# Optimization experiments

Hardware: AMD Instinct MI355X
Metric: run time of the kernel (lower is better)

The kernel has to match this reference:

```python
import jax, jax.numpy as jnp
import numpy as np
from jax import lax

B, J, I = 32, 48, 48          # batch, target len, source len
W = 2                          # target_window_size
CTX = 2 * W + 1                # 5
E, H = 128, 256                # embedding_size, hidden_units
VT, VS = 32000, 32000          # target / source vocab
S = 2 * J                      # HMM states (word + null)


def setup_inputs() -> dict:
    key = jax.random.key(0)
    ks = jax.random.split(key, 12)
    inp = {
        "target_embedding": jax.random.normal(ks[0], (VT, E), jnp.float32) * 0.02,
        "W_bridge": jax.random.normal(ks[1], (E * CTX, E), jnp.float32) * 0.02,
        "W_hidden": jax.random.normal(ks[2], (E, H), jnp.float32) * 0.02,
        "b_hidden": jnp.zeros((H,), jnp.float32),
        "W_vocab": jax.random.normal(ks[3], (H, VS), jnp.float32) * 0.02,
        "b_vocab": jnp.zeros((VS,), jnp.float32),
        "transition": jax.random.uniform(ks[4], (B, S, S), jnp.float32, 0.01, 1.0),
        "initial_transition": jax.random.uniform(ks[5], (B, S), jnp.float32, 0.01, 1.0),
        "targets_ctx": jax.random.randint(ks[6], (B, J * CTX), 0, VT, jnp.int32),
        "targets_ctx_null": jax.random.randint(ks[7], (B, J * CTX), 0, VT, jnp.int32),
        "sources": jax.random.randint(ks[8], (B, I), 0, VS, jnp.int32),
    }
    return inp


def _emission(emb, Wb, Wh, bh, Wv, bv, ctx_ids, sources):
    # embedding lookup + context reshape: [B, J*CTX, E] -> [B, J, CTX*E]
    x = emb[ctx_ids].reshape(ctx_ids.shape[0], -1, CTX * E)
    h = jnp.tanh(jnp.einsum('bjc,ce,eh->bjh', x, Wb, Wh) + bh)  # bridge+hidden
    probs = jax.nn.softmax(h @ Wv + bv, axis=-1)                # [B, J, VS]
    # per-example gather of source token columns -> [B, J, I]
    return jax.vmap(lambda p, s: p[:, s])(probs, sources)


def _forward_backward(pi, A, em):
    # pi [B,S], A [B,S,S], em [B,S,I]; scaled HMM forward-backward
    e = jnp.moveaxis(em, 2, 0)  # [I, B, S]
    a0 = pi * e[0]
    c0 = a0.sum(-1, keepdims=True)
    a0 = a0 / c0

    def fstep(a, ei):
        an = jnp.einsum('bs,bst->bt', a, A) * ei
        c = an.sum(-1, keepdims=True)
        an = an / c
        return an, (an, c)

    _, (alphas, cs) = lax.scan(fstep, a0, e[1:])
    alphas = jnp.concatenate([a0[None], alphas], 0)          # [I,B,S]
    cs = jnp.concatenate([c0[None], cs], 0)                  # [I,B,1]

    def bstep(b, inp):
        ei, ci = inp
        bn = jnp.einsum('bst,bt->bs', A, ei * b) / ci
        return bn, bn

    bI = jnp.ones_like(a0)
    _, betas_rev = lax.scan(bstep, bI, (e[1:][::-1], cs[1:][::-1]))
    betas = jnp.concatenate([betas_rev[::-1], bI[None]], 0)  # [I,B,S]

    gamma = alphas * betas                                   # state posteriors
    loglik = jnp.log(cs[..., 0]).sum(0)                      # [B]
    return jnp.moveaxis(gamma, 0, 2), loglik


def reference(target_embedding, W_bridge, W_hidden, b_hidden, W_vocab, b_vocab,
              transition, initial_transition, targets_ctx, targets_ctx_null, sources):
    em_word = _emission(target_embedding, W_bridge, W_hidden, b_hidden,
                        W_vocab, b_vocab, targets_ctx, sources)       # [B,J,I]
    em_null = _emission(target_embedding, W_bridge, W_hidden, b_hidden,
                        W_vocab, b_vocab, targets_ctx_null, sources)  # [B,J,I]
    emission = jnp.concatenate([em_word, em_null], axis=1)            # [B,2J,I]
    gamma, loglik = _forward_backward(initial_transition, transition, emission)
    return gamma, -loglik
```

## Files before the change

### kernel.cpp

```cpp
#include <hip/hip_runtime.h>
#include <hip/hip_bf16.h>

#define NB 32
#define NJ 48
#define NI 48
#define NCTX 5
#define NE 128
#define NH 256
#define NVS 32000
#define NS 96
#define NR 3072

typedef __attribute__((ext_vector_type(8))) short bf16x8;
typedef __attribute__((ext_vector_type(4))) float f32x4;

__device__ __forceinline__ unsigned short f2b(float f) {
  __hip_bfloat16 h = __float2bfloat16(f);
  return *reinterpret_cast<unsigned short*>(&h);
}
__device__ __forceinline__ float wave_sum(float v) {
  v += __shfl_xor(v, 1);
  v += __shfl_xor(v, 2);
  v += __shfl_xor(v, 4);
  v += __shfl_xor(v, 8);
  v += __shfl_xor(v, 16);
  v += __shfl_xor(v, 32);
  return v;
}
__device__ __forceinline__ void gload_lds16(const void* g, void* l) {
  __builtin_amdgcn_global_load_lds(
      (const __attribute__((address_space(1))) void*)g,
      (__attribute__((address_space(3))) void*)l, 16, 0, 0);
}

__global__ __launch_bounds__(256) void k_transpose(const float* __restrict__ Wv,
                                                   unsigned char* __restrict__ Wv8) {
  __shared__ float tile[64][65];
  int t = threadIdx.x;
  int v0 = blockIdx.x * 64, k0 = blockIdx.y * 64;
  {
    int kr = t >> 4, vq = t & 15;
#pragma unroll
    for (int it = 0; it < 4; ++it) {
      float4 v = *(const float4*)&Wv[(k0 + kr + 16 * it) * NVS + v0 + vq * 4];
      tile[kr + 16 * it][vq * 4 + 0] = v.x;
      tile[kr + 16 * it][vq * 4 + 1] = v.y;
      tile[kr + 16 * it][vq * 4 + 2] = v.z;
      tile[kr + 16 * it][vq * 4 + 3] = v.w;
    }
  }
  __syncthreads();
  {
    int vl = t >> 2, kq = t & 3;
    unsigned int q8[4];
#pragma unroll
    for (int d = 0; d < 4; ++d) {
      float f0 = tile[kq * 16 + d * 4 + 0][vl] * 64.0f;
      float f1 = tile[kq * 16 + d * 4 + 1][vl] * 64.0f;
      float f2 = tile[kq * 16 + d * 4 + 2][vl] * 64.0f;
      float f3 = tile[kq * 16 + d * 4 + 3][vl] * 64.0f;
      int w = __builtin_amdgcn_cvt_pk_fp8_f32(f0, f1, 0, false);
      w = __builtin_amdgcn_cvt_pk_fp8_f32(f2, f3, w, true);
      q8[d] = (unsigned int)w;
    }
    *(uint4*)&Wv8[(v0 + vl) * 256 + k0 + kq * 16] = *(uint4*)q8;
  }
}

__global__ __launch_bounds__(256) void k_t2b(const float* __restrict__ src,
                                             unsigned short* __restrict__ dst,
                                             int R, int C) {
  __shared__ float tile[64][65];
  int t = threadIdx.x;
  int r0 = blockIdx.x * 64, c0 = blockIdx.y * 64;
  {
    int rr = t >> 4, cq = t & 15;
#pragma unroll
    for (int it = 0; it < 4; ++it) {
      float4 v = *(const float4*)&src[(r0 + rr + 16 * it) * C + c0 + cq * 4];
      tile[rr + 16 * it][cq * 4 + 0] = v.x;
      tile[rr + 16 * it][cq * 4 + 1] = v.y;
      tile[rr + 16 * it][cq * 4 + 2] = v.z;
      tile[rr + 16 * it][cq * 4 + 3] = v.w;
    }
  }
  __syncthreads();
  {
    int cc = t >> 2, rq = t & 3;
    unsigned short pk[16];
#pragma unroll
    for (int q = 0; q < 16; ++q) pk[q] = f2b(tile[rq * 16 + q][cc]);
    *(uint4*)&dst[(c0 + cc) * R + r0 + rq * 16] = *(uint4*)&pk[0];
    *(uint4*)&dst[(c0 + cc) * R + r0 + rq * 16 + 8] = *(uint4*)&pk[8];
  }
}

__global__ __launch_bounds__(256) void k_xb(const float* __restrict__ emb,
                                            const unsigned short* __restrict__ Wbt,
                                            const int* __restrict__ tc, const int* __restrict__ tcn,
                                            unsigned short* __restrict__ xb) {
  __shared__ unsigned short Ax[32 * 72];
  __shared__ unsigned short Bw[128 * 72];
  __shared__ unsigned short xout[32 * 136];
  int t = threadIdx.x;
  int r0 = blockIdx.x * 32;
  int wave = t >> 6, lane = t & 63;
  int wm = wave >> 1, wn = wave & 1;
  int lg = lane >> 4, lr = lane & 15;
  int arow = t >> 3, aseg = t & 7;
  int r = r0 + arow;
  int half = r / 1536, rem = r % 1536, bb = rem / 48, jj = rem % 48;
  const int* ids = half ? tcn : tc;
  int brow = t >> 1, bseg = t & 1;

  f32x4 acc[4];
#pragma unroll
  for (int n = 0; n < 4; ++n) acc[n] = (f32x4){0.f, 0.f, 0.f, 0.f};

  for (int step = 0; step < 10; ++step) {
    int k0 = step * 64;
    int p = step >> 1;
    int e0 = (step & 1) * 64;
    {
      int id = ids[bb * 240 + jj * 5 + p];
      const float4* er = (const float4*)&emb[id * 128 + e0 + aseg * 8];
      float4 v0 = er[0], v1 = er[1];
      unsigned short pk[8];
      pk[0] = f2b(v0.x); pk[1] = f2b(v0.y); pk[2] = f2b(v0.z); pk[3] = f2b(v0.w);
      pk[4] = f2b(v1.x); pk[5] = f2b(v1.y); pk[6] = f2b(v1.z); pk[7] = f2b(v1.w);
      *(uint4*)&Ax[arow * 72 + aseg * 8] = *(uint4*)&pk[0];
    }
    {
      const uint4* wp = (const uint4*)&Wbt[brow * 640 + k0 + bseg * 32];
      uint4* dp = (uint4*)&Bw[brow * 72 + bseg * 32];
      uint4 w0 = wp[0], w1 = wp[1], w2 = wp[2], w3 = wp[3];
      dp[0] = w0; dp[1] = w1; dp[2] = w2; dp[3] = w3;
    }
    __syncthreads();
#pragma unroll
    for (int kk = 0; kk < 2; ++kk) {
      bf16x8 a = *(const bf16x8*)&Ax[(wm * 16 + lr) * 72 + kk * 32 + lg * 8];
#pragma unroll
      for (int n = 0; n < 4; ++n) {
        bf16x8 b = *(const bf16x8*)&Bw[(wn * 64 + n * 16 + lr) * 72 + kk * 32 + lg * 8];
        acc[n] = __builtin_amdgcn_mfma_f32_16x16x32_bf16(a, b, acc[n], 0, 0, 0);
      }
    }
    __syncthreads();
  }
#pragma unroll
  for (int n = 0; n < 4; ++n)
#pragma unroll
    for (int g = 0; g < 4; ++g)
      xout[(wm * 16 + lg * 4 + g) * 136 + wn * 64 + n * 16 + lr] = f2b(acc[n][g]);
  __syncthreads();
  {
    int orow = t >> 3, os = t & 7;
    *(uint4*)&xb[(r0 + orow) * 128 + os * 16] = *(uint4*)&xout[orow * 136 + os * 16];
    *(uint4*)&xb[(r0 + orow) * 128 + os * 16 + 8] = *(uint4*)&xout[orow * 136 + os * 16 + 8];
  }
}

__global__ __launch_bounds__(256) void k_h(const unsigned short* __restrict__ xb,
                                           const unsigned short* __restrict__ Wht,
                                           const float* __restrict__ bh,
                                           unsigned char* __restrict__ hb8) {
  __shared__ char smem[69632];
  unsigned short* Asm = (unsigned short*)smem;
  unsigned short* Bsm = (unsigned short*)(smem + 34816);
  unsigned char* o8 = (unsigned char*)smem;
  int t = threadIdx.x;
  int r0 = blockIdx.x * 128, n0 = blockIdx.y * 128;
  int wave = t >> 6, lane = t & 63;
  int wm = wave >> 1, wn = wave & 1;
  int lg = lane >> 4, lr = lane & 15;
  {
    int row = t >> 1, seg = t & 1;
#pragma unroll
    for (int i = 0; i < 8; ++i) {
      *(uint4*)&Asm[row * 136 + seg * 64 + i * 8] = *(const uint4*)&xb[(r0 + row) * 128 + seg * 64 + i * 8];
      *(uint4*)&Bsm[row * 136 + seg * 64 + i * 8] = *(const uint4*)&Wht[(n0 + row) * 128 + seg * 64 + i * 8];
    }
  }
  __syncthreads();
  f32x4 acc[4][4];
#pragma unroll
  for (int m = 0; m < 4; ++m)
#pragma unroll
    for (int n = 0; n < 4; ++n) acc[m][n] = (f32x4){0.f, 0.f, 0.f, 0.f};
#pragma unroll
  for (int kk = 0; kk < 4; ++kk) {
    bf16x8 a[4], b[4];
#pragma unroll
    for (int m = 0; m < 4; ++m)
      a[m] = *(const bf16x8*)&Asm[(wm * 64 + m * 16 + lr) * 136 + kk * 32 + lg * 8];
#pragma unroll
    for (int n = 0; n < 4; ++n)
      b[n] = *(const bf16x8*)&Bsm[(wn * 64 + n * 16 + lr) * 136 + kk * 32 + lg * 8];
#pragma unroll
    for (int m = 0; m < 4; ++m)
#pragma unroll
      for (int n = 0; n < 4; ++n)
        acc[m][n] = __builtin_amdgcn_mfma_f32_16x16x32_bf16(a[m], b[n], acc[m][n], 0, 0, 0);
  }
  __syncthreads();
#pragma unroll
  for (int n = 0; n < 4; ++n) {
    int cl = wn * 64 + n * 16 + lr;
    float bvv = bh[n0 + cl];
#pragma unroll
    for (int m = 0; m < 4; ++m) {
#pragma unroll
      for (int g = 0; g < 4; ++g) {
        int rl = wm * 64 + m * 16 + lg * 4 + g;
        float hv = tanhf(acc[m][n][g] + bvv);
        int p8 = __builtin_amdgcn_cvt_pk_fp8_f32(hv * 256.0f, 0.0f, 0, false);
        o8[rl * 144 + cl] = (unsigned char)(p8 & 0xFF);
      }
    }
  }
  __syncthreads();
  {
    int row = t >> 1, seg = t & 1;
#pragma unroll
    for (int i = 0; i < 4; ++i)
      *(uint4*)&hb8[(r0 + row) * 256 + n0 + seg * 64 + i * 16] = *(uint4*)&o8[row * 144 + seg * 64 + i * 16];
  }
}

__global__ __launch_bounds__(256) void k_denom(const unsigned char* __restrict__ hb8,
                                               const unsigned char* __restrict__ Wv8,
                                               const float* __restrict__ bv,
                                               float* __restrict__ dpart) {
  __shared__ __align__(16) unsigned char Asm[32768];
  __shared__ __align__(16) unsigned char Bsm[2][8192];
  __shared__ float red2[2][128];
  int t = threadIdx.x;
  int bid = blockIdx.x;
  int xcd = bid & 7;
  int pos = bid >> 3;
  int tile = xcd * 375 + pos;
  int vtp = tile / 24, rt = tile % 24;
  int r0 = rt * 128;
  int wave = t >> 6, lane = t & 63;
  int wm = wave >> 1, wn = wave & 1;
  int lg = lane >> 4, lr = lane & 15;

  {
    int rloc = lane >> 4, seg = lane & 15;
#pragma unroll
    for (int c = 0; c < 8; ++c) {
      int chunk = wave * 8 + c;
      int row = chunk * 4 + rloc;
      int gseg = seg ^ (row & 15);
      gload_lds16(&hb8[(r0 + row) * 256 + gseg * 16], &Asm[chunk * 1024]);
    }
  }
  int brloc = lane >> 2, bseg = lane & 3;
#pragma unroll
  for (int c = 0; c < 2; ++c) {
    int i = wave * 2 + c;
    int row = i * 16 + brloc;
    int gseg = bseg ^ ((row >> 1) & 3);
    gload_lds16(&Wv8[(vtp * 256 + row) * 256 + 0 * 64 + gseg * 16], &Bsm[0][i * 1024]);
  }
  __syncthreads();

  const float SC = 6.103515625e-05f;
  f32x4 acc[4][4];
#pragma unroll
  for (int m = 0; m < 4; ++m)
#pragma unroll
    for (int n = 0; n < 4; ++n) acc[m][n] = (f32x4){0.f, 0.f, 0.f, 0.f};

#pragma unroll
  for (int step = 0; step < 8; ++step) {
    int vt = step >> 2, ks = step & 3, buf = step & 1;
    if (step < 7) {
      int ns = step + 1;
      int nvt = ns >> 2, nks = ns & 3, nbuf = ns & 1;
#pragma unroll
      for (int c = 0; c < 2; ++c) {
        int i = wave * 2 + c;
        int row = i * 16 + brloc;
        int gseg = bseg ^ ((row >> 1) & 3);
        gload_lds16(&Wv8[((vtp * 2 + nvt) * 128 + row) * 256 + nks * 64 + gseg * 16],
                    &Bsm[nbuf][i * 1024]);
      }
    }
#pragma unroll
    for (int kk = 0; kk < 2; ++kk) {
      int lsa = ks * 4 + kk * 2 + (lg >> 1);
      int sb = kk * 2 + (lg >> 1);
      int hb = (lg & 1) << 3;
      long long a[4], b[4];
#pragma unroll
      for (int m = 0; m < 4; ++m) {
        int rr = wm * 64 + m * 16 + lr;
        a[m] = *(const long long*)&Asm[rr * 256 + ((lsa ^ lr) << 4) + hb];
      }
#pragma unroll
      for (int n = 0; n < 4; ++n) {
        int rr = wn * 64 + n * 16 + lr;
        b[n] = *(const long long*)&Bsm[buf][rr * 64 + ((sb ^ ((rr >> 1) & 3)) << 4) + hb];
      }
#pragma unroll
      for (int m = 0; m < 4; ++m)
#pragma unroll
        for (int n = 0; n < 4; ++n)
          acc[m][n] = __builtin_amdgcn_mfma_f32_16x16x32_fp8_fp8(a[m], b[n], acc[m][n], 0, 0, 0);
    }
    if (ks == 3) {
      int v0 = (vtp * 2 + vt) * 128;
      float rs[4][4];
#pragma unroll
      for (int m = 0; m < 4; ++m)
#pragma unroll
        for (int g = 0; g < 4; ++g) rs[m][g] = 0.f;
#pragma unroll
      for (int m = 0; m < 4; ++m) {
#pragma unroll
        for (int n = 0; n < 4; ++n) {
          float bvv = bv[v0 + wn * 64 + n * 16 + lr];
#pragma unroll
          for (int g = 0; g < 4; ++g) rs[m][g] += __expf(acc[m][n][g] * SC + bvv);
          acc[m][n] = (f32x4){0.f, 0.f, 0.f, 0.f};
        }
      }
#pragma unroll
      for (int m = 0; m < 4; ++m)
#pragma unroll
        for (int g = 0; g < 4; ++g) {
          float v = rs[m][g];
          v += __shfl_xor(v, 1);
          v += __shfl_xor(v, 2);
          v += __shfl_xor(v, 4);
          v += __shfl_xor(v, 8);
          rs[m][g] = v;
        }
      if (lr == 0) {
#pragma unroll
        for (int m = 0; m < 4; ++m)
#pragma unroll
          for (int g = 0; g < 4; ++g)
            red2[wn][wm * 64 + m * 16 + lg * 4 + g] = rs[m][g];
      }
      __syncthreads();
      if (t < 128) dpart[(vtp * 2 + vt) * NR + r0 + t] = red2[0][t] + red2[1][t];
    } else {
      __syncthreads();
    }
  }
}

__global__ void k_reduce(const float* __restrict__ dpart, float* __restrict__ dsum) {
  int r = blockIdx.x * 256 + threadIdx.x;
  float s = 0.f;
  for (int vt = 0; vt < 250; ++vt) s += dpart[vt * NR + r];
  dsum[r] = s;
}

__global__ __launch_bounds__(64) void k_emis(const unsigned char* __restrict__ hb8,
                                             const unsigned char* __restrict__ Wv8,
                                             const float* __restrict__ bv,
                                             const float* __restrict__ dsum,
                                             const int* __restrict__ src,
                                             float* __restrict__ em) {
  __shared__ unsigned char A8[48 * 256];
  __shared__ unsigned char B8[48 * 256];
  int t = threadIdx.x;
  int bh = blockIdx.x;
  int b = bh & 31, half = bh >> 5;
  int row4 = t >> 4, seg = t & 15;
  int rbase = half * 1536 + b * 48;
#pragma unroll
  for (int c = 0; c < 12; ++c) {
    int row = c * 4 + row4;
    int gseg = seg ^ (row & 15);
    gload_lds16(&hb8[(rbase + row) * 256 + gseg * 16], &A8[c * 1024]);
    int sv = src[b * 48 + row];
    gload_lds16(&Wv8[sv * 256 + gseg * 16], &B8[c * 1024]);
  }
  __syncthreads();
  int lg = t >> 4, lr = t & 15;
  f32x4 acc[3][3];
#pragma unroll
  for (int m = 0; m < 3; ++m)
#pragma unroll
    for (int n = 0; n < 3; ++n) acc[m][n] = (f32x4){0.f, 0.f, 0.f, 0.f};
#pragma unroll
  for (int kk = 0; kk < 8; ++kk) {
    long long a[3], bb[3];
#pragma unroll
    for (int m = 0; m < 3; ++m) {
      int rr = m * 16 + lr;
      int off = rr * 256 + ((((kk << 1) | (lg >> 1)) ^ (rr & 15)) << 4) + ((lg & 1) << 3);
      a[m] = *(const long long*)&A8[off];
      bb[m] = *(const long long*)&B8[off];
    }
#pragma unroll
    for (int m = 0; m < 3; ++m)
#pragma unroll
      for (int n = 0; n < 3; ++n)
        acc[m][n] = __builtin_amdgcn_mfma_f32_16x16x32_fp8_fp8(a[m], bb[n], acc[m][n], 0, 0, 0);
  }
  const float SC = 6.103515625e-05f;
#pragma unroll
  for (int n = 0; n < 3; ++n) {
    int i = n * 16 + lr;
    int sv = src[b * 48 + i];
    float bvv = bv[sv];
#pragma unroll
    for (int m = 0; m < 3; ++m) {
#pragma unroll
      for (int g = 0; g < 4; ++g) {
        int j = m * 16 + lg * 4 + g;
        float val = __expf(acc[m][n][g] * SC + bvv) / dsum[rbase + j];
        em[b * 4608 + (half * 48 + j) * 48 + i] = val;
      }
    }
  }
}

__global__ __launch_bounds__(192) void k_fb(const float* __restrict__ Atr, const float* __restrict__ pi,
                                            const float* __restrict__ em, float* __restrict__ alph,
                                            float* __restrict__ betas, float* __restrict__ out1) {
  __shared__ float A_st[96 * 97];
  __shared__ float em_lds[48 * 97];
  __shared__ __align__(16) float vec_lds[96];
  __shared__ float red[3];
  int t = threadIdx.x;
  int bid = blockIdx.x;
  int b = bid & 31;
  int role = bid >> 5;
  int col = t >> 1, half = t & 1;
  int base = b * 4608;

  for (int idx = t; idx < 96 * 96; idx += 192) {
    int s = idx / 96, tt = idx % 96;
    A_st[s * 97 + tt] = Atr[b * 9216 + idx];
  }
  for (int idx = t; idx < 96 * 48; idx += 192) {
    int s = idx / 48, i = idx % 48;
    em_lds[i * 97 + s] = em[base + idx];
  }
  __syncthreads();

  float Areg[48];
  if (role == 0) {
#pragma unroll
    for (int ss = 0; ss < 48; ++ss) Areg[ss] = A_st[(half * 48 + ss) * 97 + col];

    float llsum;
    {
      float v = pi[b * 96 + col] * em_lds[0 * 97 + col];
      float ws = half ? 0.f : v;
      ws = wave_sum(ws);
      if ((t & 63) == 0) red[t >> 6] = ws;
      __syncthreads();
      float c = red[0] + red[1] + red[2];
      float a = v / c;
      if (!half) {
        vec_lds[col] = a;
        alph[base + col] = a;
      }
      llsum = logf(c);
      __syncthreads();
    }
    for (int i = 1; i < 48; ++i) {
      float p = 0.f;
      const float4* ap = (const float4*)&vec_lds[half * 48];
#pragma unroll
      for (int q = 0; q < 12; ++q) {
        float4 av = ap[q];
        p += av.x * Areg[4 * q] + av.y * Areg[4 * q + 1] + av.z * Areg[4 * q + 2] + av.w * Areg[4 * q + 3];
      }
      p += __shfl_xor(p, 1);
      float an = p * em_lds[i * 97 + col];
      float ws = half ? 0.f : an;
      ws = wave_sum(ws);
      if ((t & 63) == 0) red[t >> 6] = ws;
      __syncthreads();
      float c = red[0] + red[1] + red[2];
      float a = an / c;
      if (!half) {
        vec_lds[col] = a;
        alph[base + i * 96 + col] = a;
      }
      llsum += logf(c);
      __syncthreads();
    }
    if (t == 0) out1[b] = -llsum;
  } else {
#pragma unroll
    for (int tt = 0; tt < 48; ++tt) Areg[tt] = A_st[col * 97 + half * 48 + tt];

    if (!half) {
      betas[base + 47 * 96 + col] = 1.0f;
      vec_lds[col] = em_lds[47 * 97 + col];
    }
    __syncthreads();
    for (int i = 46; i >= 0; --i) {
      float p = 0.f;
      const float4* ep = (const float4*)&vec_lds[half * 48];
#pragma unroll
      for (int q = 0; q < 12; ++q) {
        float4 ev = ep[q];
        p += ev.x * Areg[4 * q] + ev.y * Areg[4 * q + 1] + ev.z * Areg[4 * q + 2] + ev.w * Areg[4 * q + 3];
      }
      p += __shfl_xor(p, 1);
      float ws = half ? 0.f : p;
      ws = wave_sum(ws);
      if ((t & 63) == 0) red[t >> 6] = ws;
      __syncthreads();
      float c = red[0] + red[1] + red[2];
      float bt = p / c;
      if (!half) {
        betas[base + i * 96 + col] = bt;
        vec_lds[col] = em_lds[i * 97 + col] * bt;
      }
      __syncthreads();
    }
  }
}

__global__ __launch_bounds__(128) void k_gamma(const float* __restrict__ alph,
                                               const float* __restrict__ betas,
                                               float* __restrict__ out0) {
  __shared__ float red[2];
  int b = blockIdx.x, i = blockIdx.y;
  int t = threadIdx.x;
  float g = 0.f;
  if (t < 96) g = alph[b * 4608 + i * 96 + t] * betas[b * 4608 + i * 96 + t];
  float ws = wave_sum(g);
  if ((t & 63) == 0) red[t >> 6] = ws;
  __syncthreads();
  float c = red[0] + red[1];
  if (t < 96) out0[b * 4608 + t * 48 + i] = g / c;
}

extern "C" void kernel_launch(void* const* d_in, const int* in_sizes, int n_in,
                              void* d_out, int out_size, void* d_ws, size_t ws_size,
                              hipStream_t stream) {
  const float* emb = (const float*)d_in[0];
  const float* Wb  = (const float*)d_in[1];
  const float* Wh  = (const float*)d_in[2];
  const float* bh  = (const float*)d_in[3];
  const float* Wv  = (const float*)d_in[4];
  const float* bv  = (const float*)d_in[5];
  const float* Atr = (const float*)d_in[6];
  const float* pi  = (const float*)d_in[7];
  const int* tc    = (const int*)d_in[8];
  const int* tcn   = (const int*)d_in[9];
  const int* src   = (const int*)d_in[10];

  float* out0 = (float*)d_out;
  float* out1 = out0 + NB * NS * NI;

  char* ws = (char*)d_ws;
  unsigned char* wv8 = (unsigned char*)(ws);
  unsigned char* hb8 = (unsigned char*)(ws + 8192000);
  float* dpart       = (float*)(ws + 8978432);
  float* betas       = (float*)(ws + 8978432);
  float* dsum        = (float*)(ws + 12050432);
  float* em          = (float*)(ws + 12062720);
  float* alph        = (float*)(ws + 12652544);
  unsigned short* wbt = (unsigned short*)(ws + 13242368);
  unsigned short* wht = (unsigned short*)(ws + 13406208);
  unsigned short* xb  = (unsigned short*)(ws + 13471744);

  k_transpose<<<dim3(500, 4), 256, 0, stream>>>(Wv, wv8);
  k_t2b<<<dim3(10, 2), 256, 0, stream>>>(Wb, wbt, 640, 128);
  k_t2b<<<dim3(2, 4), 256, 0, stream>>>(Wh, wht, 128, 256);
  k_xb<<<96, 256, 0, stream>>>(emb, wbt, tc, tcn, xb);
  k_h<<<dim3(24, 2), 256, 0, stream>>>(xb, wht, bh, hb8);
  k_denom<<<3000, 256, 0, stream>>>(hb8, wv8, bv, dpart);
  k_reduce<<<12, 256, 0, stream>>>(dpart, dsum);
  k_emis<<<64, 64, 0, stream>>>(hb8, wv8, bv, dsum, src, em);
  k_fb<<<64, 192, 0, stream>>>(Atr, pi, em, alph, betas, out1);
  k_gamma<<<dim3(32, 48), 128, 0, stream>>>(alph, betas, out0);
}
```

Before: 159.9 us.

## Pre-swizzle fp8 operands in global memory and keep A tile in registers

The producer kernels now write Wv8 and hb8 with an 8-byte-granular XOR swizzle baked into global memory. The GEMM kernels can therefore issue linear global_load_lds copies and still read LDS without bank conflicts. k_denom loads the whole A tile into registers once instead of re-reading it from LDS every step, overlaps the reduction scratch with the A region, and raises wave priority around the MFMA bursts. k_emis caches source ids in shared memory. These changes cost extra register pressure and couple the global data layout tightly to the consumer kernels.

```diff
diff --git a/kernel.cpp b/kernel.cpp
--- a/kernel.cpp
+++ b/kernel.cpp
@@ -33,6 +33,7 @@
       (__attribute__((address_space(3))) void*)l, 16, 0, 0);
 }
 
+
 __global__ __launch_bounds__(256) void k_transpose(const float* __restrict__ Wv,
                                                    unsigned char* __restrict__ Wv8) {
   __shared__ float tile[64][65];
@@ -63,7 +64,14 @@
       w = __builtin_amdgcn_cvt_pk_fp8_f32(f2, f3, w, true);
       q8[d] = (unsigned int)w;
     }
-    *(uint4*)&Wv8[(v0 + vl) * 256 + k0 + kq * 16] = *(uint4*)q8;
+    int kqp = kq ^ ((vl >> 2) & 3);
+    unsigned int q8s[4];
+    if ((vl >> 1) & 1) {
+      q8s[0] = q8[2]; q8s[1] = q8[3]; q8s[2] = q8[0]; q8s[3] = q8[1];
+    } else {
+      q8s[0] = q8[0]; q8s[1] = q8[1]; q8s[2] = q8[2]; q8s[3] = q8[3];
+    }
+    *(uint4*)&Wv8[(v0 + vl) * 256 + k0 + kqp * 16] = *(uint4*)q8s;
   }
 }
 
@@ -222,9 +230,17 @@
   __syncthreads();
   {
     int row = t >> 1, seg = t & 1;
-#pragma unroll
-    for (int i = 0; i < 4; ++i)
-      *(uint4*)&hb8[(r0 + row) * 256 + n0 + seg * 64 + i * 16] = *(uint4*)&o8[row * 144 + seg * 64 + i * 16];
+    int sig = (row >> 1) & 7;
+    int swp = row & 1;
+#pragma unroll
+    for (int i = 0; i < 4; ++i) {
+      int p_loc = seg * 4 + i;
+      int w_loc = p_loc ^ sig;
+      unsigned long long q[2];
+      q[0] = *(const unsigned long long*)&o8[row * 144 + w_loc * 16 + swp * 8];
+      q[1] = *(const unsigned long long*)&o8[row * 144 + w_loc * 16 + (swp ^ 1) * 8];
+      *(uint4*)&hb8[(r0 + row) * 256 + n0 + p_loc * 16] = *(uint4*)q;
+    }
   }
 }
 
@@ -232,9 +248,10 @@
                                                const unsigned char* __restrict__ Wv8,
                                                const float* __restrict__ bv,
                                                float* __restrict__ dpart) {
-  __shared__ __align__(16) unsigned char Asm[32768];
-  __shared__ __align__(16) unsigned char Bsm[2][8192];
-  __shared__ float red2[2][128];
+  __shared__ __align__(16) unsigned char smem[49152];
+  unsigned char* Asm = smem;
+  float* red2 = (float*)smem;
+  unsigned char* bufp[2] = {smem + 32768, smem + 40960};
   int t = threadIdx.x;
   int bid = blockIdx.x;
   int xcd = bid & 7;
@@ -246,25 +263,30 @@
   int wm = wave >> 1, wn = wave & 1;
   int lg = lane >> 4, lr = lane & 15;
 
-  {
-    int rloc = lane >> 4, seg = lane & 15;
-#pragma unroll
-    for (int c = 0; c < 8; ++c) {
-      int chunk = wave * 8 + c;
-      int row = chunk * 4 + rloc;
-      int gseg = seg ^ (row & 15);
-      gload_lds16(&hb8[(r0 + row) * 256 + gseg * 16], &Asm[chunk * 1024]);
-    }
-  }
-  int brloc = lane >> 2, bseg = lane & 3;
+#pragma unroll
+  for (int c = 0; c < 8; ++c) {
+    int inst = wave * 8 + c;
+    gload_lds16(&hb8[(r0 + inst * 4 + (lane >> 4)) * 256 + (lane & 15) * 16], &Asm[inst * 1024]);
+  }
 #pragma unroll
   for (int c = 0; c < 2; ++c) {
     int i = wave * 2 + c;
-    int row = i * 16 + brloc;
-    int gseg = bseg ^ ((row >> 1) & 3);
-    gload_lds16(&Wv8[(vtp * 256 + row) * 256 + 0 * 64 + gseg * 16], &Bsm[0][i * 1024]);
-  }
-  __syncthreads();
+    gload_lds16(&Wv8[(vtp * 256 + i * 16 + (lane >> 2)) * 256 + 0 * 64 + (lane & 3) * 16],
+                bufp[0] + i * 1024);
+  }
+  __syncthreads();
+
+  long long a_reg[4][8];
+#pragma unroll
+  for (int m = 0; m < 4; ++m) {
+    int rowb = (wm * 64 + m * 16 + lr) * 256;
+#pragma unroll
+    for (int ks = 0; ks < 4; ++ks)
+#pragma unroll
+      for (int kk = 0; kk < 2; ++kk)
+        a_reg[m][ks * 2 + kk] =
+            *(const long long*)&Asm[rowb + (((ks * 8 + kk * 4 + lg) ^ lr) << 3)];
+  }
 
   const float SC = 6.103515625e-05f;
   f32x4 acc[4][4];
@@ -278,37 +300,31 @@
     int vt = step >> 2, ks = step & 3, buf = step & 1;
     if (step < 7) {
       int ns = step + 1;
-      int nvt = ns >> 2, nks = ns & 3, nbuf = ns & 1;
+      int nvt = ns >> 2, nks = ns & 3;
+      int vb2 = (vtp * 2 + nvt) * 128;
 #pragma unroll
       for (int c = 0; c < 2; ++c) {
         int i = wave * 2 + c;
-        int row = i * 16 + brloc;
-        int gseg = bseg ^ ((row >> 1) & 3);
-        gload_lds16(&Wv8[((vtp * 2 + nvt) * 128 + row) * 256 + nks * 64 + gseg * 16],
-                    &Bsm[nbuf][i * 1024]);
+        gload_lds16(&Wv8[(vb2 + i * 16 + (lane >> 2)) * 256 + nks * 64 + (lane & 3) * 16],
+                    bufp[buf ^ 1] + i * 1024);
       }
     }
 #pragma unroll
     for (int kk = 0; kk < 2; ++kk) {
-      int lsa = ks * 4 + kk * 2 + (lg >> 1);
-      int sb = kk * 2 + (lg >> 1);
-      int hb = (lg & 1) << 3;
-      long long a[4], b[4];
-#pragma unroll
-      for (int m = 0; m < 4; ++m) {
-        int rr = wm * 64 + m * 16 + lr;
-        a[m] = *(const long long*)&Asm[rr * 256 + ((lsa ^ lr) << 4) + hb];
-      }
+      long long b[4];
 #pragma unroll
       for (int n = 0; n < 4; ++n) {
         int rr = wn * 64 + n * 16 + lr;
-        b[n] = *(const long long*)&Bsm[buf][rr * 64 + ((sb ^ ((rr >> 1) & 3)) << 4) + hb];
-      }
+        b[n] = *(const long long*)&bufp[buf][rr * 64 + (((kk * 4 + lg) ^ ((rr >> 1) & 7)) << 3)];
+      }
+      __builtin_amdgcn_s_setprio(1);
 #pragma unroll
       for (int m = 0; m < 4; ++m)
 #pragma unroll
         for (int n = 0; n < 4; ++n)
-          acc[m][n] = __builtin_amdgcn_mfma_f32_16x16x32_fp8_fp8(a[m], b[n], acc[m][n], 0, 0, 0);
+          acc[m][n] = __builtin_amdgcn_mfma_f32_16x16x32_fp8_fp8(a_reg[m][ks * 2 + kk], b[n],
+                                                                 acc[m][n], 0, 0, 0);
+      __builtin_amdgcn_s_setprio(0);
     }
     if (ks == 3) {
       int v0 = (vtp * 2 + vt) * 128;
@@ -343,10 +359,10 @@
         for (int m = 0; m < 4; ++m)
 #pragma unroll
           for (int g = 0; g < 4; ++g)
-            red2[wn][wm * 64 + m * 16 + lg * 4 + g] = rs[m][g];
-      }
-      __syncthreads();
-      if (t < 128) dpart[(vtp * 2 + vt) * NR + r0 + t] = red2[0][t] + red2[1][t];
+            red2[wn * 128 + wm * 64 + m * 16 + lg * 4 + g] = rs[m][g];
+      }
+      __syncthreads();
+      if (t < 128) dpart[(vtp * 2 + vt) * NR + r0 + t] = red2[t] + red2[128 + t];
     } else {
       __syncthreads();
     }
@@ -368,21 +384,25 @@
                                              float* __restrict__ em) {
   __shared__ unsigned char A8[48 * 256];
   __shared__ unsigned char B8[48 * 256];
+  __shared__ int s_src[48];
   int t = threadIdx.x;
   int bh = blockIdx.x;
   int b = bh & 31, half = bh >> 5;
   int row4 = t >> 4, seg = t & 15;
   int rbase = half * 1536 + b * 48;
+  if (t < 48) s_src[t] = src[b * 48 + t];
 #pragma unroll
   for (int c = 0; c < 12; ++c) {
     int row = c * 4 + row4;
-    int gseg = seg ^ (row & 15);
-    gload_lds16(&hb8[(rbase + row) * 256 + gseg * 16], &A8[c * 1024]);
+    gload_lds16(&hb8[(rbase + row) * 256 + seg * 16], &A8[c * 1024]);
     int sv = src[b * 48 + row];
-    gload_lds16(&Wv8[sv * 256 + gseg * 16], &B8[c * 1024]);
+    gload_lds16(&Wv8[sv * 256 + seg * 16], &B8[c * 1024]);
   }
   __syncthreads();
   int lg = t >> 4, lr = t & 15;
+  int svr[3];
+#pragma unroll
+  for (int m = 0; m < 3; ++m) svr[m] = s_src[m * 16 + lr];
   f32x4 acc[3][3];
 #pragma unroll
   for (int m = 0; m < 3; ++m)
@@ -390,13 +410,14 @@
     for (int n = 0; n < 3; ++n) acc[m][n] = (f32x4){0.f, 0.f, 0.f, 0.f};
 #pragma unroll
   for (int kk = 0; kk < 8; ++kk) {
+    int sa = kk * 4 + lg;
     long long a[3], bb[3];
 #pragma unroll
     for (int m = 0; m < 3; ++m) {
       int rr = m * 16 + lr;
-      int off = rr * 256 + ((((kk << 1) | (lg >> 1)) ^ (rr & 15)) << 4) + ((lg & 1) << 3);
-      a[m] = *(const long long*)&A8[off];
-      bb[m] = *(const long long*)&B8[off];
+      a[m] = *(const long long*)&A8[rr * 256 + ((sa ^ lr) << 3)];
+      bb[m] = *(const long long*)&B8[rr * 256 + ((sa >> 3) << 6) +
+                                     (((sa & 7) ^ ((svr[m] >> 1) & 7)) << 3)];
     }
 #pragma unroll
     for (int m = 0; m < 3; ++m)
@@ -408,8 +429,7 @@
 #pragma unroll
   for (int n = 0; n < 3; ++n) {
     int i = n * 16 + lr;
-    int sv = src[b * 48 + i];
-    float bvv = bv[sv];
+    float bvv = bv[svr[n]];
 #pragma unroll
     for (int m = 0; m < 3; ++m) {
 #pragma unroll
```

After: 150.3 us. -6.0%, faster.
